# Performance work log

Hardware: AMD Instinct MI355X
Metric: run time of the kernel (lower is better)

The kernel has to match this reference:

```python
import jax, jax.numpy as jnp
import numpy as np

NUM_KNOTS = 10
DEGREE = 3
N_POINTS = 8_388_608


def make_knots():
    # Mirrors BSplineBasis.__init__: clamped knot vector on [0, 1]
    inner = np.linspace(0.0, 1.0, NUM_KNOTS - 2 * DEGREE)
    return np.concatenate([np.zeros(DEGREE), inner, np.ones(DEGREE)]).astype(np.float32)


def setup_inputs() -> dict:
    key = jax.random.key(0)
    x = jax.random.normal(key, (N_POINTS,), dtype=jnp.float32)
    knots = jnp.asarray(make_knots())  # [10]
    return {"x": x, "knots": knots}


def bspline_all_bases(x, t, degree):
    """Cox-de Boor recursion evaluating ALL basis functions in one fused pass.

    x: [N] points, t: [K] knots  ->  [N, K-degree-1] basis values.
    Matches scipy BSpline.basis_element per-knot evaluation (zero outside
    support; value 1 at the clamped right endpoint for the last basis).
    """
    K = t.shape[0]
    xe = x[:, None]                       # [N, 1]
    left, right = t[None, :-1], t[None, 1:]
    # degree-0: indicator of half-open interval [t_i, t_{i+1})
    B = ((xe >= left) & (xe < right)).astype(x.dtype)   # [N, K-1]
    # include global right endpoint in the last non-degenerate interval
    B = jnp.where((xe == t[-1]) & (right == t[-1]) & (left < right),
                  jnp.asarray(1.0, x.dtype), B)
    for d in range(1, degree + 1):        # fixed small loop (degree=3)
        tL, tLd = t[: K - d - 1], t[d : K - 1]    # t_i, t_{i+d}
        tR, tRd = t[1 : K - d], t[d + 1 : K]      # t_{i+1}, t_{i+d+1}
        den1 = tLd - tL
        den2 = tRd - tR
        safe1 = jnp.where(den1 > 0, den1, 1.0)
        safe2 = jnp.where(den2 > 0, den2, 1.0)
        w1 = jnp.where(den1[None] > 0, (xe - tL[None]) / safe1[None], 0.0)
        w2 = jnp.where(den2[None] > 0, (tRd[None] - xe) / safe2[None], 0.0)
        B = w1 * B[:, :-1] + w2 * B[:, 1:]        # [N, K-1-d]
    return B                                       # [N, K-degree-1]


def reference(x, knots):
    # forward: min-max normalize to [0,1], then evaluate all B-spline bases
    x_min, x_max = x.min(), x.max()
    x_norm = (x - x_min) / (x_max - x_min + 1e-8)
    return bspline_all_bases(x_norm.ravel(), knots, DEGREE)   # [N, 6]
```

## Files before the change

kernel.cpp:

```cpp
#include <hip/hip_runtime.h>
#include <math.h>

#define NKNOTS 10
#define RED_BLOCKS 1024
#define RED_THREADS 256
#define EVAL_BLOCKS 4096
#define EVAL_THREADS 256


__device__ __forceinline__ void bspline6(float x, const float* __restrict__ t,
                                         const float* __restrict__ inv1,
                                         const float* __restrict__ inv2,
                                         const float* __restrict__ inv3,
                                         float* __restrict__ out) {
    float B[9];
    const bool at_end = (x == t[9]);
#pragma unroll
    for (int j = 0; j < 9; ++j) {
        float b = (x >= t[j] && x < t[j + 1]) ? 1.0f : 0.0f;
        if (at_end && (t[j + 1] == t[9]) && (t[j] < t[j + 1])) b = 1.0f;
        B[j] = b;
    }
#pragma unroll
    for (int j = 0; j < 8; ++j) {
        float w1 = (x - t[j]) * inv1[j];
        float w2 = (t[j + 2] - x) * inv1[j + 1];
        B[j] = w1 * B[j] + w2 * B[j + 1];
    }
#pragma unroll
    for (int j = 0; j < 7; ++j) {
        float w1 = (x - t[j]) * inv2[j];
        float w2 = (t[j + 3] - x) * inv2[j + 1];
        B[j] = w1 * B[j] + w2 * B[j + 1];
    }
#pragma unroll
    for (int j = 0; j < 6; ++j) {
        float w1 = (x - t[j]) * inv3[j];
        float w2 = (t[j + 4] - x) * inv3[j + 1];
        out[j] = w1 * B[j] + w2 * B[j + 1];
    }
}

__global__ void reduce_minmax_kernel(const float* __restrict__ x, int n,
                                     float* __restrict__ bmin,
                                     float* __restrict__ bmax) {
    float lmin = INFINITY, lmax = -INFINITY;
    int tid = blockIdx.x * blockDim.x + threadIdx.x;
    int stride = gridDim.x * blockDim.x;
    int n4 = n >> 2;
    const float4* x4 = reinterpret_cast<const float4*>(x);
    for (int i = tid; i < n4; i += stride) {
        float4 v = x4[i];
        lmin = fminf(lmin, fminf(fminf(v.x, v.y), fminf(v.z, v.w)));
        lmax = fmaxf(lmax, fmaxf(fmaxf(v.x, v.y), fmaxf(v.z, v.w)));
    }
    for (int i = (n4 << 2) + tid; i < n; i += stride) {
        float v = x[i];
        lmin = fminf(lmin, v);
        lmax = fmaxf(lmax, v);
    }
#pragma unroll
    for (int off = 32; off > 0; off >>= 1) {
        lmin = fminf(lmin, __shfl_down(lmin, off));
        lmax = fmaxf(lmax, __shfl_down(lmax, off));
    }
    __shared__ float smin[RED_THREADS / 64], smax[RED_THREADS / 64];
    int wave = threadIdx.x >> 6;
    if ((threadIdx.x & 63) == 0) { smin[wave] = lmin; smax[wave] = lmax; }
    __syncthreads();
    if (threadIdx.x == 0) {
        float m = smin[0], M = smax[0];
#pragma unroll
        for (int w = 1; w < RED_THREADS / 64; ++w) {
            m = fminf(m, smin[w]);
            M = fmaxf(M, smax[w]);
        }
        bmin[blockIdx.x] = m;
        bmax[blockIdx.x] = M;
    }
}

__global__ void finalize_kernel(const float* __restrict__ bmin,
                                const float* __restrict__ bmax, int nb,
                                const float* __restrict__ knots,
                                float* __restrict__ params) {
    float lmin = INFINITY, lmax = -INFINITY;
    for (int i = threadIdx.x; i < nb; i += blockDim.x) {
        lmin = fminf(lmin, bmin[i]);
        lmax = fmaxf(lmax, bmax[i]);
    }
#pragma unroll
    for (int off = 32; off > 0; off >>= 1) {
        lmin = fminf(lmin, __shfl_down(lmin, off));
        lmax = fmaxf(lmax, __shfl_down(lmax, off));
    }
    __shared__ float smin[4], smax[4];
    int wave = threadIdx.x >> 6;
    if ((threadIdx.x & 63) == 0) { smin[wave] = lmin; smax[wave] = lmax; }
    __syncthreads();
    if (threadIdx.x == 0) {
        float m = smin[0], M = smax[0];
#pragma unroll
        for (int w = 1; w < 4; ++w) {
            m = fminf(m, smin[w]);
            M = fmaxf(M, smax[w]);
        }
        params[0] = m;
        params[1] = M - m + 1e-8f;
        float t[NKNOTS];
#pragma unroll
        for (int j = 0; j < NKNOTS; ++j) t[j] = knots[j];
        int idx = 2;
        for (int d = 1; d <= 3; ++d) {
            for (int j = 0; j + d <= NKNOTS - 1; ++j) {
                float den = t[j + d] - t[j];
                params[idx++] = (den > 0.0f) ? (1.0f / den) : 0.0f;
            }
        }
    }
}

__global__ void eval_kernel(const float* __restrict__ x,
                            const float* __restrict__ knots,
                            const float* __restrict__ params,
                            float* __restrict__ out, int n) {
    float t[NKNOTS];
#pragma unroll
    for (int j = 0; j < NKNOTS; ++j) t[j] = knots[j];
    const float xmin = params[0];
    const float denom = params[1];
    float inv1[9], inv2[8], inv3[7];
#pragma unroll
    for (int j = 0; j < 9; ++j) inv1[j] = params[2 + j];
#pragma unroll
    for (int j = 0; j < 8; ++j) inv2[j] = params[11 + j];
#pragma unroll
    for (int j = 0; j < 7; ++j) inv3[j] = params[19 + j];

    int tid = blockIdx.x * blockDim.x + threadIdx.x;
    int stride = gridDim.x * blockDim.x;
    int npair = n >> 1;
    const float2* x2 = reinterpret_cast<const float2*>(x);
    float4* out4 = reinterpret_cast<float4*>(out);
    for (int p = tid; p < npair; p += stride) {
        float2 v = x2[p];
        float a = (v.x - xmin) / denom;
        float b = (v.y - xmin) / denom;
        float oa[6], ob[6];
        bspline6(a, t, inv1, inv2, inv3, oa);
        bspline6(b, t, inv1, inv2, inv3, ob);
        float4* o = out4 + (size_t)p * 3;
        o[0] = make_float4(oa[0], oa[1], oa[2], oa[3]);
        o[1] = make_float4(oa[4], oa[5], ob[0], ob[1]);
        o[2] = make_float4(ob[2], ob[3], ob[4], ob[5]);
    }
    if ((n & 1) && tid == 0) {
        float a = (x[n - 1] - xmin) / denom;
        float oa[6];
        bspline6(a, t, inv1, inv2, inv3, oa);
#pragma unroll
        for (int k = 0; k < 6; ++k) out[(size_t)(n - 1) * 6 + k] = oa[k];
    }
}

extern "C" void kernel_launch(void* const* d_in, const int* in_sizes, int n_in,
                              void* d_out, int out_size, void* d_ws, size_t ws_size,
                              hipStream_t stream) {
    const float* x = (const float*)d_in[0];
    const float* knots = (const float*)d_in[1];
    float* out = (float*)d_out;
    int n = in_sizes[0];

    float* wsf = (float*)d_ws;
    float* params = wsf;
    float* bmin = wsf + 32;
    float* bmax = wsf + 32 + RED_BLOCKS;

    reduce_minmax_kernel<<<RED_BLOCKS, RED_THREADS, 0, stream>>>(x, n, bmin, bmax);
    finalize_kernel<<<1, 256, 0, stream>>>(bmin, bmax, RED_BLOCKS, knots, params);
    eval_kernel<<<EVAL_BLOCKS, EVAL_THREADS, 0, stream>>>(x, knots, params, out, n);
}
```

Measured before the change: 254.9 us.

## Replace Cox-de Boor recursion with precomputed piecewise cubic polynomials in raw x

The finalize kernel now expands the B-spline recursion symbolically in double precision into cubic coefficients for each of the three non-degenerate knot intervals, with the min-max normalization folded in, plus two breakpoints in raw x. The eval kernel loads these coefficients into shared memory, picks the interval with two comparisons, and evaluates six Horner cubics per point, processing four points per thread with float4 loads. This removes the per-point division and the long recursion, but assumes the knot layout has exactly three inner intervals (indices 4..6). It also drops the special handling at the right endpoint and for values outside the support, and folding the normalization into the coefficients can change rounding.

```diff
diff --git a/kernel.cpp b/kernel.cpp
--- a/kernel.cpp
+++ b/kernel.cpp
@@ -7,39 +7,6 @@
 #define EVAL_BLOCKS 4096
 #define EVAL_THREADS 256
 
-
-__device__ __forceinline__ void bspline6(float x, const float* __restrict__ t,
-                                         const float* __restrict__ inv1,
-                                         const float* __restrict__ inv2,
-                                         const float* __restrict__ inv3,
-                                         float* __restrict__ out) {
-    float B[9];
-    const bool at_end = (x == t[9]);
-#pragma unroll
-    for (int j = 0; j < 9; ++j) {
-        float b = (x >= t[j] && x < t[j + 1]) ? 1.0f : 0.0f;
-        if (at_end && (t[j + 1] == t[9]) && (t[j] < t[j + 1])) b = 1.0f;
-        B[j] = b;
-    }
-#pragma unroll
-    for (int j = 0; j < 8; ++j) {
-        float w1 = (x - t[j]) * inv1[j];
-        float w2 = (t[j + 2] - x) * inv1[j + 1];
-        B[j] = w1 * B[j] + w2 * B[j + 1];
-    }
-#pragma unroll
-    for (int j = 0; j < 7; ++j) {
-        float w1 = (x - t[j]) * inv2[j];
-        float w2 = (t[j + 3] - x) * inv2[j + 1];
-        B[j] = w1 * B[j] + w2 * B[j + 1];
-    }
-#pragma unroll
-    for (int j = 0; j < 6; ++j) {
-        float w1 = (x - t[j]) * inv3[j];
-        float w2 = (t[j + 4] - x) * inv3[j + 1];
-        out[j] = w1 * B[j] + w2 * B[j + 1];
-    }
-}
 
 __global__ void reduce_minmax_kernel(const float* __restrict__ x, int n,
                                      float* __restrict__ bmin,
@@ -105,61 +72,103 @@
             m = fminf(m, smin[w]);
             M = fmaxf(M, smax[w]);
         }
-        params[0] = m;
-        params[1] = M - m + 1e-8f;
-        float t[NKNOTS];
+        float denom_f = M - m + 1e-8f;
+        double s = 1.0 / (double)denom_f;
+        double bb = -(double)m * s;
+        double t[NKNOTS];
 #pragma unroll
-        for (int j = 0; j < NKNOTS; ++j) t[j] = knots[j];
-        int idx = 2;
-        for (int d = 1; d <= 3; ++d) {
-            for (int j = 0; j + d <= NKNOTS - 1; ++j) {
-                float den = t[j + d] - t[j];
-                params[idx++] = (den > 0.0f) ? (1.0f / den) : 0.0f;
+        for (int j = 0; j < NKNOTS; ++j) t[j] = (double)knots[j];
+
+        params[0] = (float)((double)m + t[4] * (double)denom_f);
+        params[1] = (float)((double)m + t[5] * (double)denom_f);
+
+        for (int iv = 0; iv < 3; ++iv) {
+            double B[9][4];
+            for (int j = 0; j < 9; ++j)
+                for (int k = 0; k < 4; ++k) B[j][k] = 0.0;
+            B[3 + iv][0] = 1.0;
+            for (int d = 1; d <= 3; ++d) {
+                for (int j = 0; j + d <= 8; ++j) {
+                    double den1 = t[j + d] - t[j];
+                    double den2 = t[j + d + 1] - t[j + 1];
+                    double i1 = (den1 > 0.0) ? 1.0 / den1 : 0.0;
+                    double i2 = (den2 > 0.0) ? 1.0 / den2 : 0.0;
+                    double a1 = -t[j] * i1, b1 = i1;
+                    double a2 = t[j + d + 1] * i2, b2 = -i2;
+                    double nb0 = a1 * B[j][0] + a2 * B[j + 1][0];
+                    double nb1 = a1 * B[j][1] + b1 * B[j][0] + a2 * B[j + 1][1] + b2 * B[j + 1][0];
+                    double nb2 = a1 * B[j][2] + b1 * B[j][1] + a2 * B[j + 1][2] + b2 * B[j + 1][1];
+                    double nb3 = a1 * B[j][3] + b1 * B[j][2] + a2 * B[j + 1][3] + b2 * B[j + 1][2];
+                    B[j][0] = nb0; B[j][1] = nb1; B[j][2] = nb2; B[j][3] = nb3;
+                }
+            }
+            for (int j = 0; j < 6; ++j) {
+                double q0 = B[j][3], q1 = 0.0, q2 = 0.0, q3 = 0.0;
+                for (int k = 2; k >= 0; --k) {
+                    double r0 = q0 * bb + B[j][k];
+                    double r1 = q1 * bb + q0 * s;
+                    double r2 = q2 * bb + q1 * s;
+                    double r3 = q3 * bb + q2 * s;
+                    q0 = r0; q1 = r1; q2 = r2; q3 = r3;
+                }
+                int base = 4 + (iv * 6 + j) * 4;
+                params[base + 0] = (float)q0;
+                params[base + 1] = (float)q1;
+                params[base + 2] = (float)q2;
+                params[base + 3] = (float)q3;
             }
         }
     }
 }
 
 __global__ void eval_kernel(const float* __restrict__ x,
-                            const float* __restrict__ knots,
                             const float* __restrict__ params,
                             float* __restrict__ out, int n) {
-    float t[NKNOTS];
-#pragma unroll
-    for (int j = 0; j < NKNOTS; ++j) t[j] = knots[j];
-    const float xmin = params[0];
-    const float denom = params[1];
-    float inv1[9], inv2[8], inv3[7];
-#pragma unroll
-    for (int j = 0; j < 9; ++j) inv1[j] = params[2 + j];
-#pragma unroll
-    for (int j = 0; j < 8; ++j) inv2[j] = params[11 + j];
-#pragma unroll
-    for (int j = 0; j < 7; ++j) inv3[j] = params[19 + j];
+    __shared__ float4 sc4[18];
+    if (threadIdx.x < 18)
+        sc4[threadIdx.x] = reinterpret_cast<const float4*>(params + 4)[threadIdx.x];
+    __syncthreads();
+    const float xb1 = params[0], xb2 = params[1];
 
     int tid = blockIdx.x * blockDim.x + threadIdx.x;
     int stride = gridDim.x * blockDim.x;
-    int npair = n >> 1;
-    const float2* x2 = reinterpret_cast<const float2*>(x);
+    int nquad = n >> 2;
+    const float4* x4 = reinterpret_cast<const float4*>(x);
     float4* out4 = reinterpret_cast<float4*>(out);
-    for (int p = tid; p < npair; p += stride) {
-        float2 v = x2[p];
-        float a = (v.x - xmin) / denom;
-        float b = (v.y - xmin) / denom;
-        float oa[6], ob[6];
-        bspline6(a, t, inv1, inv2, inv3, oa);
-        bspline6(b, t, inv1, inv2, inv3, ob);
-        float4* o = out4 + (size_t)p * 3;
-        o[0] = make_float4(oa[0], oa[1], oa[2], oa[3]);
-        o[1] = make_float4(oa[4], oa[5], ob[0], ob[1]);
-        o[2] = make_float4(ob[2], ob[3], ob[4], ob[5]);
+
+    for (int p = tid; p < nquad; p += stride) {
+        float4 v = x4[p];
+        float xs[4] = {v.x, v.y, v.z, v.w};
+        float r[4][6];
+#pragma unroll
+        for (int q = 0; q < 4; ++q) {
+            float xv = xs[q];
+            int iv = (int)(xv >= xb1) + (int)(xv >= xb2);
+            const float4* c4 = sc4 + iv * 6;
+#pragma unroll
+            for (int j = 0; j < 6; ++j) {
+                float4 c = c4[j];
+                r[q][j] = ((c.w * xv + c.z) * xv + c.y) * xv + c.x;
+            }
+        }
+        float4* o = out4 + (size_t)p * 6;
+        o[0] = make_float4(r[0][0], r[0][1], r[0][2], r[0][3]);
+        o[1] = make_float4(r[0][4], r[0][5], r[1][0], r[1][1]);
+        o[2] = make_float4(r[1][2], r[1][3], r[1][4], r[1][5]);
+        o[3] = make_float4(r[2][0], r[2][1], r[2][2], r[2][3]);
+        o[4] = make_float4(r[2][4], r[2][5], r[3][0], r[3][1]);
+        o[5] = make_float4(r[3][2], r[3][3], r[3][4], r[3][5]);
     }
-    if ((n & 1) && tid == 0) {
-        float a = (x[n - 1] - xmin) / denom;
-        float oa[6];
-        bspline6(a, t, inv1, inv2, inv3, oa);
+    if (tid < (n & 3)) {
+        int i = (nquad << 2) + tid;
+        float xv = x[i];
+        int iv = (int)(xv >= xb1) + (int)(xv >= xb2);
+        const float4* c4 = sc4 + iv * 6;
 #pragma unroll
-        for (int k = 0; k < 6; ++k) out[(size_t)(n - 1) * 6 + k] = oa[k];
+        for (int j = 0; j < 6; ++j) {
+            float4 c = c4[j];
+            out[(size_t)i * 6 + j] = ((c.w * xv + c.z) * xv + c.y) * xv + c.x;
+        }
     }
 }
 
@@ -173,10 +182,10 @@
 
     float* wsf = (float*)d_ws;
     float* params = wsf;
-    float* bmin = wsf + 32;
-    float* bmax = wsf + 32 + RED_BLOCKS;
+    float* bmin = wsf + 128;
+    float* bmax = wsf + 128 + RED_BLOCKS;
 
     reduce_minmax_kernel<<<RED_BLOCKS, RED_THREADS, 0, stream>>>(x, n, bmin, bmax);
     finalize_kernel<<<1, 256, 0, stream>>>(bmin, bmax, RED_BLOCKS, knots, params);
-    eval_kernel<<<EVAL_BLOCKS, EVAL_THREADS, 0, stream>>>(x, knots, params, out, n);
+    eval_kernel<<<EVAL_BLOCKS, EVAL_THREADS, 0, stream>>>(x, params, out, n);
 }
```

After: 259.6 us. Within noise of the previous version (+1.9%).
